# Optimization experiments

Measured on AMD Instinct MI355X. Metric: run time of the kernel, lower is better.

The kernel has to match this reference:

```python
import jax, jax.numpy as jnp
import numpy as np

B, Z, C, H = 4096, 128, 12, 512


def setup_inputs() -> dict:
    key = jax.random.key(0)
    ks = jax.random.split(key, 9)
    obs = jax.random.normal(ks[0], (B, Z, C), dtype=jnp.float32)
    action_count = jax.random.uniform(ks[1], (B, Z, Z), dtype=jnp.float32)
    adj_mask = jax.random.randint(ks[2], (Z, Z), 0, 2, dtype=jnp.int32)
    travel_times = jax.random.randint(ks[3], (Z, Z), 0, C, dtype=jnp.int32)
    w0 = jax.random.uniform(ks[4], (1,), dtype=jnp.float32)
    W1 = jax.random.normal(ks[5], (Z, H), dtype=jnp.float32) / np.sqrt(Z).astype(np.float32)
    b1 = jnp.zeros((H,), dtype=jnp.float32)
    W2 = jax.random.normal(ks[6], (H, H), dtype=jnp.float32) / np.sqrt(H).astype(np.float32)
    b2 = jnp.zeros((H,), dtype=jnp.float32)
    Wf = jax.random.normal(ks[7], (H, 1), dtype=jnp.float32) / np.sqrt(H).astype(np.float32)
    bf = jnp.zeros((1,), dtype=jnp.float32)
    return {"obs": obs, "action_count": action_count, "w0": w0,
            "W1": W1, "b1": b1, "W2": W2, "b2": b2, "Wf": Wf, "bf": bf,
            "adj_mask": adj_mask, "travel_times": travel_times}


def reference(obs, action_count, w0, W1, b1, W2, b2, Wf, bf, adj_mask, travel_times):
    # temporal decay weights: w[c] = exp(-w0 * c), c in [0, C)
    w = jnp.exp(-w0[0] * jnp.arange(C, dtype=jnp.float32))  # [C]
    # Fused equivalent of the per-zone loops:
    # temp[b,i,c] = obs[b,i,c] + sum_{j in adj(i), tt[j,i]==c} action_count[b,j,i]
    # next[b,i]   = sum_c temp[b,i,c] * w[c]
    #             = obs[b,i,:].w + sum_j adj[j,i]*w[tt[j,i]]*action_count[b,j,i]
    M = adj_mask.astype(jnp.float32) * w[travel_times]  # [Z, Z] edge weights j->i
    next_state_count = jnp.einsum('bic,c->bi', obs, w) + jnp.einsum('bji,ji->bi', action_count, M)
    # small MLP head
    x = jax.nn.relu(next_state_count @ W1 + b1)
    x = jax.nn.relu(x @ W2 + b2)
    symbolic_val = (x @ Wf + bf)[:, 0]  # [B]
    return symbolic_val, next_state_count
```

## Files before the change

kernel.cpp:

```cpp
#include <hip/hip_runtime.h>
#include <math.h>

#define ZZ 128
#define CC 12
#define HH 512
#define NB 4096

__global__ void k_edge_weights(const int* __restrict__ adj, const int* __restrict__ tt,
                               const float* __restrict__ w0p, float* __restrict__ M) {
    int e = blockIdx.x * blockDim.x + threadIdx.x;
    if (e < ZZ * ZZ) {
        float w0 = w0p[0];
        M[e] = adj[e] ? expf(-w0 * (float)tt[e]) : 0.f;
    }
}

__global__ void k_next(const float* __restrict__ obs, const float* __restrict__ act,
                       const float* __restrict__ M, const float* __restrict__ w0p,
                       float* __restrict__ out_next) {
    __shared__ float wsh[CC];
    int b = blockIdx.x;
    int i = threadIdx.x;
    if (i < CC) wsh[i] = expf(-w0p[0] * (float)i);
    __syncthreads();

    float acc = 0.f;
    const float* orow = obs + ((size_t)b * ZZ + i) * CC;
#pragma unroll
    for (int c = 0; c < CC; ++c) acc += orow[c] * wsh[c];

    const float* acol = act + (size_t)b * ZZ * ZZ + i;
#pragma unroll 4
    for (int j = 0; j < ZZ; ++j) acc += acol[(size_t)j * ZZ] * M[j * ZZ + i];

    out_next[(size_t)b * ZZ + i] = acc;
}

#define BM 64
#define BN 64
#define BK 32
#define LDSP 68

__global__ __launch_bounds__(256) void k_gemm(const float* __restrict__ A,
                                              const float* __restrict__ B,
                                              const float* __restrict__ bias,
                                              float* __restrict__ C,
                                              int Mdim, int Ndim, int Kdim, int doRelu) {
    __shared__ float As[BK * LDSP];
    __shared__ float Bs[BK * LDSP];
    int tid = threadIdx.x;
    int tx = tid % 16;
    int ty = tid / 16;
    int m0 = blockIdx.y * BM, n0 = blockIdx.x * BN;

    float acc[4][4] = {{0.f}};

    for (int k0 = 0; k0 < Kdim; k0 += BK) {
#pragma unroll
        for (int it = 0; it < (BM * BK) / 256; ++it) {
            int idx = tid + it * 256;
            int r = idx / BK, c = idx % BK;
            As[c * LDSP + r] = A[(size_t)(m0 + r) * Kdim + k0 + c];
        }
#pragma unroll
        for (int it = 0; it < (BK * BN) / 256; ++it) {
            int idx = tid + it * 256;
            int r = idx / BN, c = idx % BN;
            Bs[r * LDSP + c] = B[(size_t)(k0 + r) * Ndim + n0 + c];
        }
        __syncthreads();

#pragma unroll
        for (int k = 0; k < BK; ++k) {
            float4 a4 = *(const float4*)&As[k * LDSP + ty * 4];
            float4 b4 = *(const float4*)&Bs[k * LDSP + tx * 4];
            float av[4] = {a4.x, a4.y, a4.z, a4.w};
            float bv[4] = {b4.x, b4.y, b4.z, b4.w};
#pragma unroll
            for (int mi = 0; mi < 4; ++mi)
#pragma unroll
                for (int ni = 0; ni < 4; ++ni)
                    acc[mi][ni] += av[mi] * bv[ni];
        }
        __syncthreads();
    }

#pragma unroll
    for (int mi = 0; mi < 4; ++mi) {
        int row = m0 + ty * 4 + mi;
#pragma unroll
        for (int ni = 0; ni < 4; ++ni) {
            int col = n0 + tx * 4 + ni;
            float v = acc[mi][ni] + bias[col];
            if (doRelu) v = fmaxf(v, 0.f);
            C[(size_t)row * Ndim + col] = v;
        }
    }
}

__global__ void k_final(const float* __restrict__ x2, const float* __restrict__ Wf,
                        const float* __restrict__ bfp, float* __restrict__ out) {
    int wid = (blockIdx.x * blockDim.x + threadIdx.x) / 64;
    int lane = threadIdx.x % 64;
    const float* row = x2 + (size_t)wid * HH;
    float p = 0.f;
#pragma unroll
    for (int u = 0; u < HH / 64; ++u)
        p += row[u * 64 + lane] * Wf[u * 64 + lane];
#pragma unroll
    for (int off = 32; off; off >>= 1)
        p += __shfl_down(p, off);
    if (lane == 0) out[wid] = p + bfp[0];
}

extern "C" void kernel_launch(void* const* d_in, const int* in_sizes, int n_in,
                              void* d_out, int out_size, void* d_ws, size_t ws_size,
                              hipStream_t stream) {
    const float* obs = (const float*)d_in[0];
    const float* act = (const float*)d_in[1];
    const float* w0  = (const float*)d_in[2];
    const float* W1  = (const float*)d_in[3];
    const float* b1  = (const float*)d_in[4];
    const float* W2  = (const float*)d_in[5];
    const float* b2  = (const float*)d_in[6];
    const float* Wf  = (const float*)d_in[7];
    const float* bf  = (const float*)d_in[8];
    const int* adj   = (const int*)d_in[9];
    const int* tt    = (const int*)d_in[10];

    float* out = (float*)d_out;
    float* ws  = (float*)d_ws;

    float* M   = ws;
    float* x1  = ws + ZZ * ZZ;
    float* x2  = x1 + (size_t)NB * HH;
    float* nxt = out + NB;

    k_edge_weights<<<(ZZ * ZZ + 255) / 256, 256, 0, stream>>>(adj, tt, w0, M);
    k_next<<<NB, ZZ, 0, stream>>>(obs, act, M, w0, nxt);

    dim3 g1(HH / BN, NB / BM);
    k_gemm<<<g1, 256, 0, stream>>>(nxt, W1, b1, x1, NB, HH, ZZ, 1);
    k_gemm<<<g1, 256, 0, stream>>>(x1, W2, b2, x2, NB, HH, HH, 1);

    k_final<<<NB / 4, 256, 0, stream>>>(x2, Wf, bf, out);
}
```

Before: 114.9 us.

## Switch MLP GEMMs to split-bf16 MFMA and fuse final projection

Replaces the fp32 SIMT GEMMs with bf16 MFMA matrix-core GEMMs that split each fp32 value into high and low bf16 halves and use three products to keep near-fp32 accuracy. Weights are transposed and split in a prep kernel that also merges edge-weight computation and output bias initialisation. The second GEMM fuses bias, ReLU and the final Wf dot product through shuffles and atomics, so x2 is never written. The next-state kernel is vectorised with float4 loads over coalesced rows and writes the split bf16 activations directly. This adds atomic contention, a weight-conversion pass on every call, and a small precision loss.

Measured after the change: 138.7 us. 20.7% more time.

```diff
diff --git a/kernel.cpp b/kernel.cpp
--- a/kernel.cpp
+++ b/kernel.cpp
@@ -6,111 +6,207 @@
 #define HH 512
 #define NB 4096
 
-__global__ void k_edge_weights(const int* __restrict__ adj, const int* __restrict__ tt,
-                               const float* __restrict__ w0p, float* __restrict__ M) {
-    int e = blockIdx.x * blockDim.x + threadIdx.x;
-    if (e < ZZ * ZZ) {
+typedef __attribute__((ext_vector_type(8))) short short8;
+typedef __attribute__((ext_vector_type(4))) float f32x4;
+
+__device__ __forceinline__ unsigned short f2bf(float x) {
+    unsigned u = __builtin_bit_cast(unsigned, x);
+    u += 0x7FFFu + ((u >> 16) & 1u);
+    return (unsigned short)(u >> 16);
+}
+__device__ __forceinline__ float bf2f(unsigned short h) {
+    unsigned u = ((unsigned)h) << 16;
+    return __builtin_bit_cast(float, u);
+}
+
+__global__ __launch_bounds__(256) void k_prep(const float* __restrict__ W1,
+                                              const float* __restrict__ W2,
+                                              const int* __restrict__ adj,
+                                              const int* __restrict__ tt,
+                                              const float* __restrict__ w0p,
+                                              const float* __restrict__ bfp,
+                                              short* __restrict__ W1tH, short* __restrict__ W1tL,
+                                              short* __restrict__ W2tH, short* __restrict__ W2tL,
+                                              float* __restrict__ M, float* __restrict__ outv) {
+    int bid = blockIdx.x, t = threadIdx.x;
+    if (bid < 80) {
+        __shared__ float T[64][65];
+        const float* src; short *dH, *dL; int k0, n0, Krows;
+        if (bid < 64) { src = W2; dH = W2tH; dL = W2tL; Krows = HH; k0 = (bid & 7) * 64; n0 = (bid >> 3) * 64; }
+        else { int b = bid - 64; src = W1; dH = W1tH; dL = W1tL; Krows = ZZ; k0 = (b & 1) * 64; n0 = (b >> 1) * 64; }
+#pragma unroll
+        for (int it = 0; it < 16; ++it) {
+            int idx = t + it * 256; int r = idx >> 6, c = idx & 63;
+            T[r][c] = src[(size_t)(k0 + r) * HH + n0 + c];
+        }
+        __syncthreads();
+#pragma unroll
+        for (int it = 0; it < 16; ++it) {
+            int idx = t + it * 256; int nl = idx >> 6, kl = idx & 63;
+            float v = T[kl][nl];
+            unsigned short h = f2bf(v);
+            float lo = v - bf2f(h);
+            size_t o = (size_t)(n0 + nl) * Krows + k0 + kl;
+            dH[o] = (short)h; dL[o] = (short)f2bf(lo);
+        }
+    } else if (bid == 80) {
         float w0 = w0p[0];
-        M[e] = adj[e] ? expf(-w0 * (float)tt[e]) : 0.f;
-    }
-}
-
-__global__ void k_next(const float* __restrict__ obs, const float* __restrict__ act,
-                       const float* __restrict__ M, const float* __restrict__ w0p,
-                       float* __restrict__ out_next) {
-    __shared__ float wsh[CC];
-    int b = blockIdx.x;
-    int i = threadIdx.x;
-    if (i < CC) wsh[i] = expf(-w0p[0] * (float)i);
+#pragma unroll
+        for (int it = 0; it < 64; ++it) {
+            int e = t + it * 256;
+            M[e] = adj[e] ? expf(-w0 * (float)tt[e]) : 0.f;
+        }
+    } else {
+        float bv = bfp[0];
+#pragma unroll
+        for (int it = 0; it < 16; ++it) outv[t + it * 256] = bv;
+    }
+}
+
+__global__ __launch_bounds__(256) void k_next(const float* __restrict__ obs,
+                                              const float* __restrict__ act,
+                                              const float* __restrict__ M,
+                                              const float* __restrict__ w0p,
+                                              float* __restrict__ outn,
+                                              short* __restrict__ nxtH,
+                                              short* __restrict__ nxtL) {
+    __shared__ float P[2][4][128];
+    __shared__ float wsh[16];
+    int t = threadIdx.x;
+    int b0 = blockIdx.x * 2;
+    if (t < CC) wsh[t] = expf(-w0p[0] * (float)t);
+    int i4 = t & 31, jg = (t >> 5) & 3, bo = t >> 7;
+    const float* abase = act + (size_t)(b0 + bo) * ZZ * ZZ;
+    float4 acc = make_float4(0.f, 0.f, 0.f, 0.f);
+#pragma unroll 8
+    for (int jj = 0; jj < 32; ++jj) {
+        int j = jg * 32 + jj;
+        float4 a = *(const float4*)&abase[j * ZZ + i4 * 4];
+        float4 m = *(const float4*)&M[j * ZZ + i4 * 4];
+        acc.x += a.x * m.x; acc.y += a.y * m.y; acc.z += a.z * m.z; acc.w += a.w * m.w;
+    }
+    *(float4*)&P[bo][jg][i4 * 4] = acc;
     __syncthreads();
-
-    float acc = 0.f;
-    const float* orow = obs + ((size_t)b * ZZ + i) * CC;
-#pragma unroll
-    for (int c = 0; c < CC; ++c) acc += orow[c] * wsh[c];
-
-    const float* acol = act + (size_t)b * ZZ * ZZ + i;
-#pragma unroll 4
-    for (int j = 0; j < ZZ; ++j) acc += acol[(size_t)j * ZZ] * M[j * ZZ + i];
-
-    out_next[(size_t)b * ZZ + i] = acc;
-}
-
-#define BM 64
-#define BN 64
-#define BK 32
-#define LDSP 68
-
-__global__ __launch_bounds__(256) void k_gemm(const float* __restrict__ A,
-                                              const float* __restrict__ B,
+    int i = t & 127, bo2 = t >> 7;
+    int bb = b0 + bo2;
+    float s = P[bo2][0][i] + P[bo2][1][i] + P[bo2][2][i] + P[bo2][3][i];
+    const float* orow = obs + ((size_t)bb * ZZ + i) * CC;
+#pragma unroll
+    for (int c = 0; c < CC; ++c) s += orow[c] * wsh[c];
+    outn[(size_t)bb * ZZ + i] = s;
+    unsigned short h = f2bf(s);
+    nxtH[bb * ZZ + i] = (short)h;
+    nxtL[bb * ZZ + i] = (short)f2bf(s - bf2f(h));
+}
+
+#define GBM 64
+#define GBN 128
+#define GBK 64
+
+__global__ __launch_bounds__(128) void k_gemm(const short* __restrict__ Ah,
+                                              const short* __restrict__ Al,
+                                              const short* __restrict__ Bh,
+                                              const short* __restrict__ Bl,
                                               const float* __restrict__ bias,
-                                              float* __restrict__ C,
-                                              int Mdim, int Ndim, int Kdim, int doRelu) {
-    __shared__ float As[BK * LDSP];
-    __shared__ float Bs[BK * LDSP];
-    int tid = threadIdx.x;
-    int tx = tid % 16;
-    int ty = tid / 16;
-    int m0 = blockIdx.y * BM, n0 = blockIdx.x * BN;
-
-    float acc[4][4] = {{0.f}};
-
-    for (int k0 = 0; k0 < Kdim; k0 += BK) {
-#pragma unroll
-        for (int it = 0; it < (BM * BK) / 256; ++it) {
-            int idx = tid + it * 256;
-            int r = idx / BK, c = idx % BK;
-            As[c * LDSP + r] = A[(size_t)(m0 + r) * Kdim + k0 + c];
-        }
-#pragma unroll
-        for (int it = 0; it < (BK * BN) / 256; ++it) {
-            int idx = tid + it * 256;
-            int r = idx / BN, c = idx % BN;
-            Bs[r * LDSP + c] = B[(size_t)(k0 + r) * Ndim + n0 + c];
+                                              int Kdim, int mode,
+                                              short* __restrict__ OutH,
+                                              short* __restrict__ OutL,
+                                              const float* __restrict__ Wf,
+                                              float* __restrict__ OutDot) {
+    __shared__ __align__(16) short AsH[GBM * GBK], AsL[GBM * GBK];
+    __shared__ __align__(16) short BsH[GBN * GBK], BsL[GBN * GBK];
+    int t = threadIdx.x;
+    int m0 = blockIdx.y * GBM, n0 = blockIdx.x * GBN;
+    int lane = t & 63, wn = t >> 6;
+    int l15 = lane & 15, l4 = lane >> 4;
+    f32x4 acc[4][4] = {};
+
+    for (int k0 = 0; k0 < Kdim; k0 += GBK) {
+#pragma unroll
+        for (int it = 0; it < 4; ++it) {
+            int idx = t + it * 128; int row = idx >> 3, ch = idx & 7, cs = ch ^ (row & 7);
+            *(int4*)&AsH[row * GBK + cs * 8] = *(const int4*)&Ah[(size_t)(m0 + row) * Kdim + k0 + ch * 8];
+            *(int4*)&AsL[row * GBK + cs * 8] = *(const int4*)&Al[(size_t)(m0 + row) * Kdim + k0 + ch * 8];
+        }
+#pragma unroll
+        for (int it = 0; it < 8; ++it) {
+            int idx = t + it * 128; int row = idx >> 3, ch = idx & 7, cs = ch ^ (row & 7);
+            *(int4*)&BsH[row * GBK + cs * 8] = *(const int4*)&Bh[(size_t)(n0 + row) * Kdim + k0 + ch * 8];
+            *(int4*)&BsL[row * GBK + cs * 8] = *(const int4*)&Bl[(size_t)(n0 + row) * Kdim + k0 + ch * 8];
         }
         __syncthreads();
-
-#pragma unroll
-        for (int k = 0; k < BK; ++k) {
-            float4 a4 = *(const float4*)&As[k * LDSP + ty * 4];
-            float4 b4 = *(const float4*)&Bs[k * LDSP + tx * 4];
-            float av[4] = {a4.x, a4.y, a4.z, a4.w};
-            float bv[4] = {b4.x, b4.y, b4.z, b4.w};
-#pragma unroll
-            for (int mi = 0; mi < 4; ++mi)
-#pragma unroll
-                for (int ni = 0; ni < 4; ++ni)
-                    acc[mi][ni] += av[mi] * bv[ni];
+#pragma unroll
+        for (int s = 0; s < 2; ++s) {
+            short8 ah[4], al[4], bh[4], bl[4];
+            int g = s * 4 + l4;
+#pragma unroll
+            for (int mf = 0; mf < 4; ++mf) {
+                int row = mf * 16 + l15;
+                int addr = row * GBK + ((g ^ (row & 7)) << 3);
+                ah[mf] = *(const short8*)&AsH[addr];
+                al[mf] = *(const short8*)&AsL[addr];
+            }
+#pragma unroll
+            for (int nf = 0; nf < 4; ++nf) {
+                int row = wn * 64 + nf * 16 + l15;
+                int addr = row * GBK + ((g ^ (row & 7)) << 3);
+                bh[nf] = *(const short8*)&BsH[addr];
+                bl[nf] = *(const short8*)&BsL[addr];
+            }
+#pragma unroll
+            for (int mf = 0; mf < 4; ++mf)
+#pragma unroll
+                for (int nf = 0; nf < 4; ++nf) {
+                    acc[mf][nf] = __builtin_amdgcn_mfma_f32_16x16x32_bf16(ah[mf], bh[nf], acc[mf][nf], 0, 0, 0);
+                    acc[mf][nf] = __builtin_amdgcn_mfma_f32_16x16x32_bf16(ah[mf], bl[nf], acc[mf][nf], 0, 0, 0);
+                    acc[mf][nf] = __builtin_amdgcn_mfma_f32_16x16x32_bf16(al[mf], bh[nf], acc[mf][nf], 0, 0, 0);
+                }
         }
         __syncthreads();
     }
 
-#pragma unroll
-    for (int mi = 0; mi < 4; ++mi) {
-        int row = m0 + ty * 4 + mi;
-#pragma unroll
-        for (int ni = 0; ni < 4; ++ni) {
-            int col = n0 + tx * 4 + ni;
-            float v = acc[mi][ni] + bias[col];
-            if (doRelu) v = fmaxf(v, 0.f);
-            C[(size_t)row * Ndim + col] = v;
-        }
-    }
-}
-
-__global__ void k_final(const float* __restrict__ x2, const float* __restrict__ Wf,
-                        const float* __restrict__ bfp, float* __restrict__ out) {
-    int wid = (blockIdx.x * blockDim.x + threadIdx.x) / 64;
-    int lane = threadIdx.x % 64;
-    const float* row = x2 + (size_t)wid * HH;
-    float p = 0.f;
-#pragma unroll
-    for (int u = 0; u < HH / 64; ++u)
-        p += row[u * 64 + lane] * Wf[u * 64 + lane];
-#pragma unroll
-    for (int off = 32; off; off >>= 1)
-        p += __shfl_down(p, off);
-    if (lane == 0) out[wid] = p + bfp[0];
+    if (mode == 0) {
+#pragma unroll
+        for (int mf = 0; mf < 4; ++mf)
+#pragma unroll
+            for (int nf = 0; nf < 4; ++nf) {
+                int col = n0 + wn * 64 + nf * 16 + l15;
+                float bv = bias[col];
+#pragma unroll
+                for (int r = 0; r < 4; ++r) {
+                    int row = m0 + mf * 16 + l4 * 4 + r;
+                    float v = fmaxf(acc[mf][nf][r] + bv, 0.f);
+                    unsigned short h = f2bf(v);
+                    OutH[(size_t)row * HH + col] = (short)h;
+                    OutL[(size_t)row * HH + col] = (short)f2bf(v - bf2f(h));
+                }
+            }
+    } else {
+        float bv[4], wv[4];
+#pragma unroll
+        for (int nf = 0; nf < 4; ++nf) {
+            int col = n0 + wn * 64 + nf * 16 + l15;
+            bv[nf] = bias[col];
+            wv[nf] = Wf[col];
+        }
+#pragma unroll
+        for (int mf = 0; mf < 4; ++mf)
+#pragma unroll
+            for (int r = 0; r < 4; ++r) {
+                float p = 0.f;
+#pragma unroll
+                for (int nf = 0; nf < 4; ++nf)
+                    p += fmaxf(acc[mf][nf][r] + bv[nf], 0.f) * wv[nf];
+                p += __shfl_xor(p, 1);
+                p += __shfl_xor(p, 2);
+                p += __shfl_xor(p, 4);
+                p += __shfl_xor(p, 8);
+                if (l15 == 0) {
+                    int row = m0 + mf * 16 + l4 * 4 + r;
+                    atomicAdd(&OutDot[row], p);
+                }
+            }
+    }
 }
 
 extern "C" void kernel_launch(void* const* d_in, const int* in_sizes, int n_in,
@@ -129,19 +225,27 @@
     const int* tt    = (const int*)d_in[10];
 
     float* out = (float*)d_out;
-    float* ws  = (float*)d_ws;
-
-    float* M   = ws;
-    float* x1  = ws + ZZ * ZZ;
-    float* x2  = x1 + (size_t)NB * HH;
-    float* nxt = out + NB;
-
-    k_edge_weights<<<(ZZ * ZZ + 255) / 256, 256, 0, stream>>>(adj, tt, w0, M);
-    k_next<<<NB, ZZ, 0, stream>>>(obs, act, M, w0, nxt);
-
-    dim3 g1(HH / BN, NB / BM);
-    k_gemm<<<g1, 256, 0, stream>>>(nxt, W1, b1, x1, NB, HH, ZZ, 1);
-    k_gemm<<<g1, 256, 0, stream>>>(x1, W2, b2, x2, NB, HH, HH, 1);
-
-    k_final<<<NB / 4, 256, 0, stream>>>(x2, Wf, bf, out);
-}
+    float* outn = out + NB;
+
+    char* base = (char*)d_ws;
+    float* M    = (float*)base;
+    short* nxtH = (short*)(base + (1u << 16));
+    short* nxtL = (short*)(base + (1u << 16) + (1u << 20));
+    char* p = base + (1u << 16) + (2u << 20);
+    short* W1tH = (short*)p;               p += (size_t)HH * ZZ * 2;
+    short* W1tL = (short*)p;               p += (size_t)HH * ZZ * 2;
+    short* W2tH = (short*)p;               p += (size_t)HH * HH * 2;
+    short* W2tL = (short*)p;               p += (size_t)HH * HH * 2;
+    short* x1H  = (short*)p;               p += (size_t)NB * HH * 2;
+    short* x1L  = (short*)p;
+
+    k_prep<<<82, 256, 0, stream>>>(W1, W2, adj, tt, w0, bf,
+                                   W1tH, W1tL, W2tH, W2tL, M, out);
+    k_next<<<NB / 2, 256, 0, stream>>>(obs, act, M, w0, outn, nxtH, nxtL);
+
+    dim3 g(HH / GBN, NB / GBM);
+    k_gemm<<<g, 128, 0, stream>>>(nxtH, nxtL, W1tH, W1tL, b1, ZZ, 0,
+                                  x1H, x1L, (const float*)nullptr, (float*)nullptr);
+    k_gemm<<<g, 128, 0, stream>>>(x1H, x1L, W2tH, W2tL, b2, HH, 1,
+                                  (short*)nullptr, (short*)nullptr, Wf, out);
+}
```
